# Kernel optimization log

Measured on AMD Instinct MI355X. Metric: run time of the kernel, lower is better.

Reference implementation:

```python
import jax, jax.numpy as jnp
import numpy as np

N_NODES = 20000
N_EDGES = 320000
IN_F = 16
OUT_F = 16
EDGE_DIM = 16
EDGE_HID = 64
BN_EPS = 1e-5


def setup_inputs() -> dict:
    key = jax.random.key(0)
    ks = jax.random.split(key, 12)
    inp = {
        "h_neigh": jax.random.normal(ks[0], (N_NODES, IN_F), dtype=jnp.float32),
        "h_self": jax.random.normal(ks[1], (N_NODES, IN_F), dtype=jnp.float32),
        "edge_features": jax.random.normal(ks[2], (N_EDGES, EDGE_DIM), dtype=jnp.float32),
        "src": jax.random.randint(ks[3], (N_EDGES,), 0, N_NODES),
        "dst": jax.random.randint(ks[4], (N_EDGES,), 0, N_NODES),
        # params (xavier-ish scale)
        "W_self": jax.random.normal(ks[5], (IN_F, OUT_F), dtype=jnp.float32) * (2.0 / (IN_F + OUT_F)) ** 0.5,
        "bn_gamma": jnp.ones((OUT_F,), dtype=jnp.float32),
        "bn_beta": jnp.zeros((OUT_F,), dtype=jnp.float32),
        "We1": jax.random.normal(ks[6], (EDGE_DIM, EDGE_HID), dtype=jnp.float32) * (2.0 / (EDGE_DIM + EDGE_HID)) ** 0.5,
        "be1": jnp.zeros((EDGE_HID,), dtype=jnp.float32),
        "We2": jax.random.normal(ks[7], (EDGE_HID, IN_F * OUT_F), dtype=jnp.float32) * (2.0 / (EDGE_HID + IN_F * OUT_F)) ** 0.5,
        "be2": jnp.zeros((IN_F * OUT_F,), dtype=jnp.float32),
    }
    return inp


def reference(h_neigh, h_self, edge_features, src, dst,
              W_self, bn_gamma, bn_beta, We1, be1, We2, be2):
    n_nodes = h_self.shape[0]
    in_f, out_f = W_self.shape
    # edge MLP -> per-edge weight matrix [E, in_f, out_f]
    eh = jax.nn.relu(edge_features @ We1 + be1)
    edge_w = (eh @ We2 + be2).reshape(-1, in_f, out_f)
    # gather src features, per-edge matvec, scatter-sum to dst
    # (sum over in_f commutes with the edge sum-reduce, matching
    #  update_all(u_mul_e, sum) followed by .sum(dim=1))
    msg = jnp.einsum('ei,eio->eo', h_neigh[src], edge_w)  # [E, out_f]
    neigh = jax.ops.segment_sum(msg, dst, num_segments=n_nodes)  # [N, out_f]
    # fc_self: Linear(no bias) -> BatchNorm1d (training stats) -> tanh
    y = h_self @ W_self
    mu = y.mean(axis=0)
    var = y.var(axis=0)
    y = (y - mu) / jnp.sqrt(var + BN_EPS) * bn_gamma + bn_beta
    y = jnp.tanh(y)
    z = jax.nn.relu(y + neigh)
    z_norm = jnp.linalg.norm(z, axis=1, keepdims=True)
    z_norm = jnp.where(z_norm == 0, jnp.ones_like(z_norm), z_norm)
    return z / z_norm
```

## Files before the change

kernel.cpp:

```cpp
#include <hip/hip_runtime.h>
#include <hip/hip_bf16.h>
#include <math.h>

#define NN 20000
#define NE 320000
#define BN_EPS 1e-5f
#define CAP 48
#define CNTP 16

#define MSG_BYTES   (NE * 16 * 4)
#define ELIST_OFF   MSG_BYTES
#define ELIST_BYTES (NN * CAP * 4)
#define CNT_OFF     (ELIST_OFF + ELIST_BYTES)
#define CNT_BYTES   (NN * CNTP * 4)
#define BNACC_OFF   (CNT_OFF + CNT_BYTES)
#define Y_OFF       (BNACC_OFF + 128)
#define ZERO_OFF    CNT_OFF
#define ZERO_BYTES  (CNT_BYTES + 128)

typedef __bf16 bf16x8 __attribute__((ext_vector_type(8)));
typedef float  f32x4  __attribute__((ext_vector_type(4)));

union BF8 { bf16x8 v; unsigned short us[8]; unsigned int ui[4]; };

__device__ __forceinline__ unsigned short f2bf(float f) {
    unsigned int u = __builtin_bit_cast(unsigned int, f);
    u += 0x7FFFu + ((u >> 16) & 1u);
    return (unsigned short)(u >> 16);
}
__device__ __forceinline__ float bf2f(unsigned short s) {
    unsigned int u = ((unsigned int)s) << 16;
    return __builtin_bit_cast(float, u);
}
__device__ __forceinline__ unsigned int pack2bf(float a, float b) {
    return (unsigned int)f2bf(a) | ((unsigned int)f2bf(b) << 16);
}

__global__ __launch_bounds__(256, 4) void edge_kernel(
    const float* __restrict__ h_neigh, const float* __restrict__ efeat,
    const int* __restrict__ src, const int* __restrict__ dst,
    const float* __restrict__ We1, const float* __restrict__ be1,
    const float* __restrict__ We2, const float* __restrict__ be2,
    float* __restrict__ msgb, int* __restrict__ elist,
    int* __restrict__ cntp,
    const float* __restrict__ h_self, const float* __restrict__ Wsf,
    float* __restrict__ y, float* __restrict__ bnacc)
{
    __shared__ __align__(16) unsigned short A3sw[16 * 2 * 64 * 8];
    __shared__ float red[4][32];

    const int t = threadIdx.x;

    {
        const float4* W2v = (const float4*)We2;
#pragma unroll
        for (int it = 0; it < 16; it++) {
            int c4 = t + 256 * it;
            float4 w = W2v[c4];
            int f = c4 * 4;
            int h = f >> 8, c = f & 255;
            int mb = c >> 4, kb = h >> 5, hh = h & 31, co = c & 15;
            int base = ((mb * 2 + kb) * 64 + (hh >> 3) * 16) * 8 + (hh & 7);
            A3sw[base + (co + 0) * 8] = f2bf(w.x);
            A3sw[base + (co + 1) * 8] = f2bf(w.y);
            A3sw[base + (co + 2) * 8] = f2bf(w.z);
            A3sw[base + (co + 3) * 8] = f2bf(w.w);
        }
    }

    for (int i = (int)blockIdx.x * 256 + t; i < NE; i += (int)gridDim.x * 256) {
        int d0 = dst[i];
        int k0 = atomicAdd(&cntp[d0 * CNTP], 1);
        if (k0 < CAP) elist[d0 * CAP + k0] = i;
    }
    __syncthreads();

    const int L = t & 63, wv = t >> 6;
    const int lo16 = L & 15, q = L >> 4;
    const int qc = q & 1;
    const bool qlow = (q < 2);
    const bool qhi1 = ((q >> 1) != 0);

    BF8 w1h[4], w1l[4];
#pragma unroll
    for (int c = 0; c < 4; c++) {
#pragma unroll
        for (int j = 0; j < 8; j++) {
            float w;
            if (q < 2)                 w = We1[(q * 8 + j) * 64 + c * 16 + lo16];
            else if (q == 2 && j == 0) w = be1[c * 16 + lo16];
            else                       w = 0.f;
            unsigned short h = f2bf(w);
            w1h[c].us[j] = h;
            w1l[c].us[j] = f2bf(w - bf2f(h));
        }
    }

    BF8 be2T;
#pragma unroll
    for (int j = 0; j < 8; j++) {
        float bv = be2[(qc * 8 + j) * 16 + lo16];
        be2T.us[j] = qlow ? f2bf(bv) : (unsigned short)0;
    }

    const int addrA = (((q & 1) * 2 + 0) * 16 + lo16) * 4;
    const int addrB = (((q & 1) * 2 + 1) * 16 + lo16) * 4;

    const int NT = NE / 64;
    int bt = blockIdx.x;
    {
        int e = bt * 64 + wv * 16 + lo16;
        int se = src[e];

        while (true) {
            int btn = bt + gridDim.x;
            bool hn = btn < NT;
            int en = 0, sen = 0;
            if (hn) {
                en = btn * 64 + wv * 16 + lo16;
                sen = src[en];
            }

            float xr[16];
            {
                const float4* xp = (const float4*)(h_neigh + (size_t)se * 16);
#pragma unroll
                for (int k4 = 0; k4 < 4; k4++) {
                    float4 a = xp[k4];
                    xr[k4*4+0] = a.x; xr[k4*4+1] = a.y; xr[k4*4+2] = a.z; xr[k4*4+3] = a.w;
                }
            }

            BF8 a2h, a2l;
            {
                const float4* ep = (const float4*)(efeat + (size_t)e * 16 + qc * 8);
                float4 e0 = ep[0], e1 = ep[1];
                float ev[8] = {e0.x, e0.y, e0.z, e0.w, e1.x, e1.y, e1.z, e1.w};
#pragma unroll
                for (int j = 0; j < 8; j++) {
                    if (qlow) {
                        unsigned short h = f2bf(ev[j]);
                        a2h.us[j] = h;
                        a2l.us[j] = f2bf(ev[j] - bf2f(h));
                    } else {
                        a2h.us[j] = (q == 2 && j == 0) ? (unsigned short)0x3F80 : (unsigned short)0;
                        a2l.us[j] = 0;
                    }
                }
            }

            float vch[4][4];
#pragma unroll
            for (int c = 0; c < 4; c++) {
                f32x4 c2 = {0.f, 0.f, 0.f, 0.f};
                c2 = __builtin_amdgcn_mfma_f32_16x16x32_bf16(w1h[c].v, a2h.v, c2, 0, 0, 0);
                c2 = __builtin_amdgcn_mfma_f32_16x16x32_bf16(w1l[c].v, a2h.v, c2, 0, 0, 0);
                c2 = __builtin_amdgcn_mfma_f32_16x16x32_bf16(w1h[c].v, a2l.v, c2, 0, 0, 0);
#pragma unroll
                for (int r = 0; r < 4; r++) vch[c][r] = fmaxf(c2[r], 0.f);
            }

            unsigned int dwH[4][2], dwL[4][2];
#pragma unroll
            for (int c = 0; c < 4; c++) {
#pragma unroll
                for (int d = 0; d < 2; d++) {
                    float va = vch[c][2*d], vb = vch[c][2*d+1];
                    unsigned short ha = f2bf(va), hb = f2bf(vb);
                    dwH[c][d] = (unsigned int)ha | ((unsigned int)hb << 16);
                    dwL[c][d] = pack2bf(va - bf2f(ha), vb - bf2f(hb));
                }
            }

            BF8 b3h[2], b3l[2];
#pragma unroll
            for (int kb = 0; kb < 2; kb++) {
#pragma unroll
                for (int tt = 0; tt < 4; tt++) {
                    int d = tt & 1;
                    int addr = (tt >> 1) ? addrB : addrA;
                    int h0 = __builtin_amdgcn_ds_bpermute(addr, (int)dwH[kb*2+0][d]);
                    int h1 = __builtin_amdgcn_ds_bpermute(addr, (int)dwH[kb*2+1][d]);
                    int l0 = __builtin_amdgcn_ds_bpermute(addr, (int)dwL[kb*2+0][d]);
                    int l1 = __builtin_amdgcn_ds_bpermute(addr, (int)dwL[kb*2+1][d]);
                    b3h[kb].ui[tt] = (unsigned int)(qhi1 ? h1 : h0);
                    b3l[kb].ui[tt] = (unsigned int)(qhi1 ? l1 : l0);
                }
            }

            BF8 xT;
#pragma unroll
            for (int j = 0; j < 8; j++)
                xT.us[j] = qlow ? f2bf(xr[qc * 8 + j]) : (unsigned short)0;
            f32x4 msg = {0.f, 0.f, 0.f, 0.f};
            msg = __builtin_amdgcn_mfma_f32_16x16x32_bf16(be2T.v, xT.v, msg, 0, 0, 0);

#pragma unroll 4
            for (int mb = 0; mb < 16; mb++) {
                bf16x8 a3a = *(const bf16x8*)&A3sw[((mb * 2 + 0) * 64 + L) * 8];
                bf16x8 a3b = *(const bf16x8*)&A3sw[((mb * 2 + 1) * 64 + L) * 8];
                f32x4 acc = {0.f, 0.f, 0.f, 0.f};
                acc = __builtin_amdgcn_mfma_f32_16x16x32_bf16(a3a, b3h[0].v, acc, 0, 0, 0);
                acc = __builtin_amdgcn_mfma_f32_16x16x32_bf16(a3b, b3h[1].v, acc, 0, 0, 0);
                acc = __builtin_amdgcn_mfma_f32_16x16x32_bf16(a3a, b3l[0].v, acc, 0, 0, 0);
                acc = __builtin_amdgcn_mfma_f32_16x16x32_bf16(a3b, b3l[1].v, acc, 0, 0, 0);
                float xm = xr[mb];
                msg[0] += xm * acc[0];
                msg[1] += xm * acc[1];
                msg[2] += xm * acc[2];
                msg[3] += xm * acc[3];
            }

            *(float4*)(msgb + (size_t)e * 16 + q * 4) =
                make_float4(msg[0], msg[1], msg[2], msg[3]);

            if (!hn) break;
            bt = btn; e = en; se = sen;
        }
    }

    int sb = (int)blockIdx.x - 945;
    if (sb >= 0 && sb < 79) {
        int n = sb * 256 + t;
        bool act = (n < NN);
        float hv[16], yv[16];
        if (act) {
            const float4* h4 = (const float4*)(h_self + (size_t)n * 16);
#pragma unroll
            for (int k = 0; k < 4; k++) {
                float4 a = h4[k];
                hv[4*k+0] = a.x; hv[4*k+1] = a.y; hv[4*k+2] = a.z; hv[4*k+3] = a.w;
            }
        } else {
#pragma unroll
            for (int i = 0; i < 16; i++) hv[i] = 0.f;
        }
#pragma unroll
        for (int o = 0; o < 16; o++) {
            float a = 0.f;
#pragma unroll
            for (int i = 0; i < 16; i++) a += hv[i] * Wsf[i*16 + o];
            yv[o] = a;
        }
        if (act) {
            float4* y4 = (float4*)(y + (size_t)n * 16);
#pragma unroll
            for (int k = 0; k < 4; k++)
                y4[k] = make_float4(yv[4*k+0], yv[4*k+1], yv[4*k+2], yv[4*k+3]);
        }
        int lane = t & 63;
#pragma unroll
        for (int o = 0; o < 16; o++) {
            float a = act ? yv[o] : 0.f;
            float b = act ? yv[o]*yv[o] : 0.f;
#pragma unroll
            for (int off = 32; off > 0; off >>= 1) {
                a += __shfl_down(a, off);
                b += __shfl_down(b, off);
            }
            if (lane == 0) { red[wv][o] = a; red[wv][16 + o] = b; }
        }
        __syncthreads();
        if (t < 32) {
            float s = red[0][t] + red[1][t] + red[2][t] + red[3][t];
            atomicAdd(&bnacc[t], s);
        }
    }
}

__global__ __launch_bounds__(256) void final_kernel(
    const float* __restrict__ msgb, const int* __restrict__ elist,
    const int* __restrict__ cntp, const int* __restrict__ dst,
    const float* __restrict__ y, const float* __restrict__ bnacc,
    const float* __restrict__ gamma, const float* __restrict__ beta,
    float* __restrict__ out)
{
    int tb = blockIdx.x * 256 + threadIdx.x;
    int n = tb >> 2, c = tb & 3;
    if (n >= NN) return;

    int deg = cntp[n * CNTP];
    const float4* m4 = (const float4*)msgb;

    float ax = 0.f, ay = 0.f, az = 0.f, aw = 0.f;
    if (deg <= CAP) {
        const int* el = elist + n * CAP;
        int k = 0;
        for (; k + 4 <= deg; k += 4) {
            int e0 = el[k], e1 = el[k+1], e2 = el[k+2], e3 = el[k+3];
            float4 a0 = m4[(size_t)e0*4 + c];
            float4 a1 = m4[(size_t)e1*4 + c];
            float4 a2 = m4[(size_t)e2*4 + c];
            float4 a3 = m4[(size_t)e3*4 + c];
            ax += (a0.x + a1.x) + (a2.x + a3.x);
            ay += (a0.y + a1.y) + (a2.y + a3.y);
            az += (a0.z + a1.z) + (a2.z + a3.z);
            aw += (a0.w + a1.w) + (a2.w + a3.w);
        }
        for (; k < deg; k++) {
            int e0 = el[k];
            float4 a0 = m4[(size_t)e0*4 + c];
            ax += a0.x; ay += a0.y; az += a0.z; aw += a0.w;
        }
    } else {
        for (int e0 = 0; e0 < NE; e0++) {
            if (dst[e0] == n) {
                float4 a0 = m4[(size_t)e0*4 + c];
                ax += a0.x; ay += a0.y; az += a0.z; aw += a0.w;
            }
        }
    }

    float4 yv4 = ((const float4*)y)[(size_t)n * 4 + c];
    float yv[4] = {yv4.x, yv4.y, yv4.z, yv4.w};
    float nb[4] = {ax, ay, az, aw};

    const float inv_n = 1.f / (float)NN;
    float z[4];
    float ss = 0.f;
#pragma unroll
    for (int r = 0; r < 4; r++) {
        int o = c * 4 + r;
        float mu  = bnacc[o] * inv_n;
        float var = bnacc[16 + o] * inv_n - mu * mu;
        float inv = rsqrtf(var + BN_EPS);
        float yy  = (yv[r] - mu) * inv * gamma[o] + beta[o];
        float tt  = tanhf(yy);
        float zz  = fmaxf(tt + nb[r], 0.f);
        z[r] = zz;
        ss += zz * zz;
    }
    ss += __shfl_xor(ss, 1);
    ss += __shfl_xor(ss, 2);
    float nrm = sqrtf(ss);
    if (nrm == 0.f) nrm = 1.f;
    float rr = 1.f / nrm;
    *(float4*)(out + (size_t)n * 16 + c * 4) =
        make_float4(z[0]*rr, z[1]*rr, z[2]*rr, z[3]*rr);
}

extern "C" void kernel_launch(void* const* d_in, const int* in_sizes, int n_in,
                              void* d_out, int out_size, void* d_ws, size_t ws_size,
                              hipStream_t stream) {
    const float* h_neigh = (const float*)d_in[0];
    const float* h_self  = (const float*)d_in[1];
    const float* efeat   = (const float*)d_in[2];
    const int*   src     = (const int*)d_in[3];
    const int*   dst     = (const int*)d_in[4];
    const float* W_self  = (const float*)d_in[5];
    const float* gamma   = (const float*)d_in[6];
    const float* beta    = (const float*)d_in[7];
    const float* We1     = (const float*)d_in[8];
    const float* be1     = (const float*)d_in[9];
    const float* We2     = (const float*)d_in[10];
    const float* be2     = (const float*)d_in[11];
    float* out = (float*)d_out;

    char* ws = (char*)d_ws;
    float* msgb  = (float*)ws;
    int*   elist = (int*)(ws + ELIST_OFF);
    int*   cntp  = (int*)(ws + CNT_OFF);
    float* bnacc = (float*)(ws + BNACC_OFF);
    float* y     = (float*)(ws + Y_OFF);

    hipMemsetAsync(ws + ZERO_OFF, 0, ZERO_BYTES, stream);

    edge_kernel<<<1024, 256, 0, stream>>>(
        h_neigh, efeat, src, dst, We1, be1, We2, be2,
        msgb, elist, cntp,
        h_self, W_self, y, bnacc);
    final_kernel<<<(NN * 4 + 255) / 256, 256, 0, stream>>>(
        msgb, elist, cntp, dst, y, bnacc, gamma, beta, out);
}
```

Baseline: 156.3 us.

## Double edge-kernel block size, use per-wave grid-stride loop, use native bf16 conversions

The edge kernel moves from 256 to 512 threads per block, raising launch bounds to 8 waves per SIMD target, so each block's one-time LDS staging of the We2 matrix is shared by twice as many waves. The main loop changes from a per-block tile loop with software prefetch of the next src index to a simple per-wave grid-stride loop over 16-edge groups, which drops the prefetch. Bucketing by destination becomes one edge per thread, since 1024×512 threads cover all edges. The BN-statistics blocks are remapped to the last blocks. Manual bf16 round/extend bit tricks are replaced by native __bf16 casts, which may map to hardware conversion instructions. The tighter launch bound risks register spills, and losing the prefetch may expose gather latency.

```diff
diff --git a/kernel.cpp b/kernel.cpp
--- a/kernel.cpp
+++ b/kernel.cpp
@@ -24,19 +24,17 @@
 union BF8 { bf16x8 v; unsigned short us[8]; unsigned int ui[4]; };
 
 __device__ __forceinline__ unsigned short f2bf(float f) {
-    unsigned int u = __builtin_bit_cast(unsigned int, f);
-    u += 0x7FFFu + ((u >> 16) & 1u);
-    return (unsigned short)(u >> 16);
+    __bf16 h = (__bf16)f;
+    return __builtin_bit_cast(unsigned short, h);
 }
 __device__ __forceinline__ float bf2f(unsigned short s) {
-    unsigned int u = ((unsigned int)s) << 16;
-    return __builtin_bit_cast(float, u);
+    return (float)__builtin_bit_cast(__bf16, s);
 }
 __device__ __forceinline__ unsigned int pack2bf(float a, float b) {
     return (unsigned int)f2bf(a) | ((unsigned int)f2bf(b) << 16);
 }
 
-__global__ __launch_bounds__(256, 4) void edge_kernel(
+__global__ __launch_bounds__(512, 8) void edge_kernel(
     const float* __restrict__ h_neigh, const float* __restrict__ efeat,
     const int* __restrict__ src, const int* __restrict__ dst,
     const float* __restrict__ We1, const float* __restrict__ be1,
@@ -47,15 +45,15 @@
     float* __restrict__ y, float* __restrict__ bnacc)
 {
     __shared__ __align__(16) unsigned short A3sw[16 * 2 * 64 * 8];
-    __shared__ float red[4][32];
+    __shared__ float red[8][32];
 
     const int t = threadIdx.x;
 
     {
         const float4* W2v = (const float4*)We2;
 #pragma unroll
-        for (int it = 0; it < 16; it++) {
-            int c4 = t + 256 * it;
+        for (int it = 0; it < 8; it++) {
+            int c4 = t + 512 * it;
             float4 w = W2v[c4];
             int f = c4 * 4;
             int h = f >> 8, c = f & 255;
@@ -68,10 +66,13 @@
         }
     }
 
-    for (int i = (int)blockIdx.x * 256 + t; i < NE; i += (int)gridDim.x * 256) {
-        int d0 = dst[i];
-        int k0 = atomicAdd(&cntp[d0 * CNTP], 1);
-        if (k0 < CAP) elist[d0 * CAP + k0] = i;
+    {
+        int i = (int)blockIdx.x * 512 + t;
+        if (i < NE) {
+            int d0 = dst[i];
+            int k0 = atomicAdd(&cntp[d0 * CNTP], 1);
+            if (k0 < CAP) elist[d0 * CAP + k0] = i;
+        }
     }
     __syncthreads();
 
@@ -106,122 +107,109 @@
     const int addrA = (((q & 1) * 2 + 0) * 16 + lo16) * 4;
     const int addrB = (((q & 1) * 2 + 1) * 16 + lo16) * 4;
 
-    const int NT = NE / 64;
-    int bt = blockIdx.x;
-    {
-        int e = bt * 64 + wv * 16 + lo16;
+    const int NG = NE / 16;
+    const int NW = (int)gridDim.x * 8;
+    for (int g = (int)blockIdx.x * 8 + wv; g < NG; g += NW) {
+        int e = g * 16 + lo16;
         int se = src[e];
 
-        while (true) {
-            int btn = bt + gridDim.x;
-            bool hn = btn < NT;
-            int en = 0, sen = 0;
-            if (hn) {
-                en = btn * 64 + wv * 16 + lo16;
-                sen = src[en];
-            }
-
-            float xr[16];
-            {
-                const float4* xp = (const float4*)(h_neigh + (size_t)se * 16);
-#pragma unroll
-                for (int k4 = 0; k4 < 4; k4++) {
-                    float4 a = xp[k4];
-                    xr[k4*4+0] = a.x; xr[k4*4+1] = a.y; xr[k4*4+2] = a.z; xr[k4*4+3] = a.w;
+        float xr[16];
+        {
+            const float4* xp = (const float4*)(h_neigh + (size_t)se * 16);
+#pragma unroll
+            for (int k4 = 0; k4 < 4; k4++) {
+                float4 a = xp[k4];
+                xr[k4*4+0] = a.x; xr[k4*4+1] = a.y; xr[k4*4+2] = a.z; xr[k4*4+3] = a.w;
+            }
+        }
+
+        BF8 a2h, a2l;
+        {
+            const float4* ep = (const float4*)(efeat + (size_t)e * 16 + qc * 8);
+            float4 e0 = ep[0], e1 = ep[1];
+            float ev[8] = {e0.x, e0.y, e0.z, e0.w, e1.x, e1.y, e1.z, e1.w};
+#pragma unroll
+            for (int j = 0; j < 8; j++) {
+                if (qlow) {
+                    unsigned short h = f2bf(ev[j]);
+                    a2h.us[j] = h;
+                    a2l.us[j] = f2bf(ev[j] - bf2f(h));
+                } else {
+                    a2h.us[j] = (q == 2 && j == 0) ? (unsigned short)0x3F80 : (unsigned short)0;
+                    a2l.us[j] = 0;
                 }
             }
-
-            BF8 a2h, a2l;
-            {
-                const float4* ep = (const float4*)(efeat + (size_t)e * 16 + qc * 8);
-                float4 e0 = ep[0], e1 = ep[1];
-                float ev[8] = {e0.x, e0.y, e0.z, e0.w, e1.x, e1.y, e1.z, e1.w};
-#pragma unroll
-                for (int j = 0; j < 8; j++) {
-                    if (qlow) {
-                        unsigned short h = f2bf(ev[j]);
-                        a2h.us[j] = h;
-                        a2l.us[j] = f2bf(ev[j] - bf2f(h));
-                    } else {
-                        a2h.us[j] = (q == 2 && j == 0) ? (unsigned short)0x3F80 : (unsigned short)0;
-                        a2l.us[j] = 0;
-                    }
-                }
-            }
-
-            float vch[4][4];
-#pragma unroll
-            for (int c = 0; c < 4; c++) {
-                f32x4 c2 = {0.f, 0.f, 0.f, 0.f};
-                c2 = __builtin_amdgcn_mfma_f32_16x16x32_bf16(w1h[c].v, a2h.v, c2, 0, 0, 0);
-                c2 = __builtin_amdgcn_mfma_f32_16x16x32_bf16(w1l[c].v, a2h.v, c2, 0, 0, 0);
-                c2 = __builtin_amdgcn_mfma_f32_16x16x32_bf16(w1h[c].v, a2l.v, c2, 0, 0, 0);
-#pragma unroll
-                for (int r = 0; r < 4; r++) vch[c][r] = fmaxf(c2[r], 0.f);
-            }
-
-            unsigned int dwH[4][2], dwL[4][2];
-#pragma unroll
-            for (int c = 0; c < 4; c++) {
-#pragma unroll
-                for (int d = 0; d < 2; d++) {
-                    float va = vch[c][2*d], vb = vch[c][2*d+1];
-                    unsigned short ha = f2bf(va), hb = f2bf(vb);
-                    dwH[c][d] = (unsigned int)ha | ((unsigned int)hb << 16);
-                    dwL[c][d] = pack2bf(va - bf2f(ha), vb - bf2f(hb));
-                }
-            }
-
-            BF8 b3h[2], b3l[2];
-#pragma unroll
-            for (int kb = 0; kb < 2; kb++) {
-#pragma unroll
-                for (int tt = 0; tt < 4; tt++) {
-                    int d = tt & 1;
-                    int addr = (tt >> 1) ? addrB : addrA;
-                    int h0 = __builtin_amdgcn_ds_bpermute(addr, (int)dwH[kb*2+0][d]);
-                    int h1 = __builtin_amdgcn_ds_bpermute(addr, (int)dwH[kb*2+1][d]);
-                    int l0 = __builtin_amdgcn_ds_bpermute(addr, (int)dwL[kb*2+0][d]);
-                    int l1 = __builtin_amdgcn_ds_bpermute(addr, (int)dwL[kb*2+1][d]);
-                    b3h[kb].ui[tt] = (unsigned int)(qhi1 ? h1 : h0);
-                    b3l[kb].ui[tt] = (unsigned int)(qhi1 ? l1 : l0);
-                }
-            }
-
-            BF8 xT;
-#pragma unroll
-            for (int j = 0; j < 8; j++)
-                xT.us[j] = qlow ? f2bf(xr[qc * 8 + j]) : (unsigned short)0;
-            f32x4 msg = {0.f, 0.f, 0.f, 0.f};
-            msg = __builtin_amdgcn_mfma_f32_16x16x32_bf16(be2T.v, xT.v, msg, 0, 0, 0);
+        }
+
+        float vch[4][4];
+#pragma unroll
+        for (int c = 0; c < 4; c++) {
+            f32x4 c2 = {0.f, 0.f, 0.f, 0.f};
+            c2 = __builtin_amdgcn_mfma_f32_16x16x32_bf16(w1h[c].v, a2h.v, c2, 0, 0, 0);
+            c2 = __builtin_amdgcn_mfma_f32_16x16x32_bf16(w1l[c].v, a2h.v, c2, 0, 0, 0);
+            c2 = __builtin_amdgcn_mfma_f32_16x16x32_bf16(w1h[c].v, a2l.v, c2, 0, 0, 0);
+#pragma unroll
+            for (int r = 0; r < 4; r++) vch[c][r] = fmaxf(c2[r], 0.f);
+        }
+
+        unsigned int dwH[4][2], dwL[4][2];
+#pragma unroll
+        for (int c = 0; c < 4; c++) {
+#pragma unroll
+            for (int d = 0; d < 2; d++) {
+                float va = vch[c][2*d], vb = vch[c][2*d+1];
+                unsigned short ha = f2bf(va), hb = f2bf(vb);
+                dwH[c][d] = (unsigned int)ha | ((unsigned int)hb << 16);
+                dwL[c][d] = pack2bf(va - bf2f(ha), vb - bf2f(hb));
+            }
+        }
+
+        BF8 b3h[2], b3l[2];
+#pragma unroll
+        for (int kb = 0; kb < 2; kb++) {
+#pragma unroll
+            for (int tt = 0; tt < 4; tt++) {
+                int d = tt & 1;
+                int addr = (tt >> 1) ? addrB : addrA;
+                int h0 = __builtin_amdgcn_ds_bpermute(addr, (int)dwH[kb*2+0][d]);
+                int h1 = __builtin_amdgcn_ds_bpermute(addr, (int)dwH[kb*2+1][d]);
+                int l0 = __builtin_amdgcn_ds_bpermute(addr, (int)dwL[kb*2+0][d]);
+                int l1 = __builtin_amdgcn_ds_bpermute(addr, (int)dwL[kb*2+1][d]);
+                b3h[kb].ui[tt] = (unsigned int)(qhi1 ? h1 : h0);
+                b3l[kb].ui[tt] = (unsigned int)(qhi1 ? l1 : l0);
+            }
+        }
+
+        BF8 xT;
+#pragma unroll
+        for (int j = 0; j < 8; j++)
+            xT.us[j] = qlow ? f2bf(xr[qc * 8 + j]) : (unsigned short)0;
+        f32x4 msg = {0.f, 0.f, 0.f, 0.f};
+        msg = __builtin_amdgcn_mfma_f32_16x16x32_bf16(be2T.v, xT.v, msg, 0, 0, 0);
 
 #pragma unroll 4
-            for (int mb = 0; mb < 16; mb++) {
-                bf16x8 a3a = *(const bf16x8*)&A3sw[((mb * 2 + 0) * 64 + L) * 8];
-                bf16x8 a3b = *(const bf16x8*)&A3sw[((mb * 2 + 1) * 64 + L) * 8];
-                f32x4 acc = {0.f, 0.f, 0.f, 0.f};
-                acc = __builtin_amdgcn_mfma_f32_16x16x32_bf16(a3a, b3h[0].v, acc, 0, 0, 0);
-                acc = __builtin_amdgcn_mfma_f32_16x16x32_bf16(a3b, b3h[1].v, acc, 0, 0, 0);
-                acc = __builtin_amdgcn_mfma_f32_16x16x32_bf16(a3a, b3l[0].v, acc, 0, 0, 0);
-                acc = __builtin_amdgcn_mfma_f32_16x16x32_bf16(a3b, b3l[1].v, acc, 0, 0, 0);
-                float xm = xr[mb];
-                msg[0] += xm * acc[0];
-                msg[1] += xm * acc[1];
-                msg[2] += xm * acc[2];
-                msg[3] += xm * acc[3];
-            }
-
-            *(float4*)(msgb + (size_t)e * 16 + q * 4) =
-                make_float4(msg[0], msg[1], msg[2], msg[3]);
-
-            if (!hn) break;
-            bt = btn; e = en; se = sen;
-        }
-    }
-
-    int sb = (int)blockIdx.x - 945;
-    if (sb >= 0 && sb < 79) {
-        int n = sb * 256 + t;
+        for (int mb = 0; mb < 16; mb++) {
+            bf16x8 a3a = *(const bf16x8*)&A3sw[((mb * 2 + 0) * 64 + L) * 8];
+            bf16x8 a3b = *(const bf16x8*)&A3sw[((mb * 2 + 1) * 64 + L) * 8];
+            f32x4 acc = {0.f, 0.f, 0.f, 0.f};
+            acc = __builtin_amdgcn_mfma_f32_16x16x32_bf16(a3a, b3h[0].v, acc, 0, 0, 0);
+            acc = __builtin_amdgcn_mfma_f32_16x16x32_bf16(a3b, b3h[1].v, acc, 0, 0, 0);
+            acc = __builtin_amdgcn_mfma_f32_16x16x32_bf16(a3a, b3l[0].v, acc, 0, 0, 0);
+            acc = __builtin_amdgcn_mfma_f32_16x16x32_bf16(a3b, b3l[1].v, acc, 0, 0, 0);
+            float xm = xr[mb];
+            msg[0] += xm * acc[0];
+            msg[1] += xm * acc[1];
+            msg[2] += xm * acc[2];
+            msg[3] += xm * acc[3];
+        }
+
+        *(float4*)(msgb + (size_t)e * 16 + q * 4) =
+            make_float4(msg[0], msg[1], msg[2], msg[3]);
+    }
+
+    int sb = (int)blockIdx.x - 984;
+    if (sb >= 0) {
+        int n = sb * 512 + t;
         bool act = (n < NN);
         float hv[16], yv[16];
         if (act) {
@@ -262,7 +250,9 @@
         }
         __syncthreads();
         if (t < 32) {
-            float s = red[0][t] + red[1][t] + red[2][t] + red[3][t];
+            float s = 0.f;
+#pragma unroll
+            for (int w = 0; w < 8; w++) s += red[w][t];
             atomicAdd(&bnacc[t], s);
         }
     }
@@ -365,7 +355,7 @@
 
     hipMemsetAsync(ws + ZERO_OFF, 0, ZERO_BYTES, stream);
 
-    edge_kernel<<<1024, 256, 0, stream>>>(
+    edge_kernel<<<1024, 512, 0, stream>>>(
         h_neigh, efeat, src, dst, We1, be1, We2, be2,
         msgb, elist, cntp,
         h_self, W_self, y, bnacc);
```

Result: slower. 196.9 us (+26.0%).

## Switch edge MLP MFMAs from split-bf16 to single fp16

Applied to the files above, without the earlier changes.

Replaces the hi/lo bf16 splitting, which took three or four MFMAs per product plus extra bpermutes, with single fp16 MFMAs. This roughly halves the matrix work and the cross-lane shuffles in the edge MLP. The first four We2 tiles are also held in registers instead of being reloaded from LDS on every iteration. fp16 has a narrower range and gives less precision than the split-bf16 scheme, and the register-cached tiles raise register pressure.

```diff
diff --git a/kernel.cpp b/kernel.cpp
--- a/kernel.cpp
+++ b/kernel.cpp
@@ -18,22 +18,17 @@
 #define ZERO_OFF    CNT_OFF
 #define ZERO_BYTES  (CNT_BYTES + 128)
 
-typedef __bf16 bf16x8 __attribute__((ext_vector_type(8)));
-typedef float  f32x4  __attribute__((ext_vector_type(4)));
-
-union BF8 { bf16x8 v; unsigned short us[8]; unsigned int ui[4]; };
-
-__device__ __forceinline__ unsigned short f2bf(float f) {
-    unsigned int u = __builtin_bit_cast(unsigned int, f);
-    u += 0x7FFFu + ((u >> 16) & 1u);
-    return (unsigned short)(u >> 16);
-}
-__device__ __forceinline__ float bf2f(unsigned short s) {
-    unsigned int u = ((unsigned int)s) << 16;
-    return __builtin_bit_cast(float, u);
-}
-__device__ __forceinline__ unsigned int pack2bf(float a, float b) {
-    return (unsigned int)f2bf(a) | ((unsigned int)f2bf(b) << 16);
+typedef _Float16 f16x8 __attribute__((ext_vector_type(8)));
+typedef float    f32x4 __attribute__((ext_vector_type(4)));
+
+union H8 { f16x8 v; unsigned short us[8]; unsigned int ui[4]; };
+
+__device__ __forceinline__ unsigned short f2h(float f) {
+    _Float16 h = (_Float16)f;
+    return __builtin_bit_cast(unsigned short, h);
+}
+__device__ __forceinline__ unsigned int pack2h(float a, float b) {
+    return (unsigned int)f2h(a) | ((unsigned int)f2h(b) << 16);
 }
 
 __global__ __launch_bounds__(256, 4) void edge_kernel(
@@ -61,10 +56,10 @@
             int h = f >> 8, c = f & 255;
             int mb = c >> 4, kb = h >> 5, hh = h & 31, co = c & 15;
             int base = ((mb * 2 + kb) * 64 + (hh >> 3) * 16) * 8 + (hh & 7);
-            A3sw[base + (co + 0) * 8] = f2bf(w.x);
-            A3sw[base + (co + 1) * 8] = f2bf(w.y);
-            A3sw[base + (co + 2) * 8] = f2bf(w.z);
-            A3sw[base + (co + 3) * 8] = f2bf(w.w);
+            A3sw[base + (co + 0) * 8] = f2h(w.x);
+            A3sw[base + (co + 1) * 8] = f2h(w.y);
+            A3sw[base + (co + 2) * 8] = f2h(w.z);
+            A3sw[base + (co + 3) * 8] = f2h(w.w);
         }
     }
 
@@ -81,7 +76,14 @@
     const bool qlow = (q < 2);
     const bool qhi1 = ((q >> 1) != 0);
 
-    BF8 w1h[4], w1l[4];
+    H8 a3r[4][2];
+#pragma unroll
+    for (int mb = 0; mb < 4; mb++) {
+        a3r[mb][0].v = *(const f16x8*)&A3sw[((mb * 2 + 0) * 64 + L) * 8];
+        a3r[mb][1].v = *(const f16x8*)&A3sw[((mb * 2 + 1) * 64 + L) * 8];
+    }
+
+    H8 w1[4];
 #pragma unroll
     for (int c = 0; c < 4; c++) {
 #pragma unroll
@@ -90,17 +92,15 @@
             if (q < 2)                 w = We1[(q * 8 + j) * 64 + c * 16 + lo16];
             else if (q == 2 && j == 0) w = be1[c * 16 + lo16];
             else                       w = 0.f;
-            unsigned short h = f2bf(w);
-            w1h[c].us[j] = h;
-            w1l[c].us[j] = f2bf(w - bf2f(h));
-        }
-    }
-
-    BF8 be2T;
+            w1[c].us[j] = f2h(w);
+        }
+    }
+
+    H8 be2T;
 #pragma unroll
     for (int j = 0; j < 8; j++) {
         float bv = be2[(qc * 8 + j) * 16 + lo16];
-        be2T.us[j] = qlow ? f2bf(bv) : (unsigned short)0;
+        be2T.us[j] = qlow ? f2h(bv) : (unsigned short)0;
     }
 
     const int addrA = (((q & 1) * 2 + 0) * 16 + lo16) * 4;
@@ -131,7 +131,7 @@
                 }
             }
 
-            BF8 a2h, a2l;
+            H8 a2;
             {
                 const float4* ep = (const float4*)(efeat + (size_t)e * 16 + qc * 8);
                 float4 e0 = ep[0], e1 = ep[1];
@@ -139,12 +139,9 @@
 #pragma unroll
                 for (int j = 0; j < 8; j++) {
                     if (qlow) {
-                        unsigned short h = f2bf(ev[j]);
-                        a2h.us[j] = h;
-                        a2l.us[j] = f2bf(ev[j] - bf2f(h));
+                        a2.us[j] = f2h(ev[j]);
                     } else {
-                        a2h.us[j] = (q == 2 && j == 0) ? (unsigned short)0x3F80 : (unsigned short)0;
-                        a2l.us[j] = 0;
+                        a2.us[j] = (q == 2 && j == 0) ? (unsigned short)0x3C00 : (unsigned short)0;
                     }
                 }
             }
@@ -153,57 +150,57 @@
 #pragma unroll
             for (int c = 0; c < 4; c++) {
                 f32x4 c2 = {0.f, 0.f, 0.f, 0.f};
-                c2 = __builtin_amdgcn_mfma_f32_16x16x32_bf16(w1h[c].v, a2h.v, c2, 0, 0, 0);
-                c2 = __builtin_amdgcn_mfma_f32_16x16x32_bf16(w1l[c].v, a2h.v, c2, 0, 0, 0);
-                c2 = __builtin_amdgcn_mfma_f32_16x16x32_bf16(w1h[c].v, a2l.v, c2, 0, 0, 0);
+                c2 = __builtin_amdgcn_mfma_f32_16x16x32_f16(w1[c].v, a2.v, c2, 0, 0, 0);
 #pragma unroll
                 for (int r = 0; r < 4; r++) vch[c][r] = fmaxf(c2[r], 0.f);
             }
 
-            unsigned int dwH[4][2], dwL[4][2];
+            unsigned int dw[4][2];
 #pragma unroll
             for (int c = 0; c < 4; c++) {
 #pragma unroll
-                for (int d = 0; d < 2; d++) {
-                    float va = vch[c][2*d], vb = vch[c][2*d+1];
-                    unsigned short ha = f2bf(va), hb = f2bf(vb);
-                    dwH[c][d] = (unsigned int)ha | ((unsigned int)hb << 16);
-                    dwL[c][d] = pack2bf(va - bf2f(ha), vb - bf2f(hb));
-                }
-            }
-
-            BF8 b3h[2], b3l[2];
+                for (int d = 0; d < 2; d++)
+                    dw[c][d] = pack2h(vch[c][2*d], vch[c][2*d+1]);
+            }
+
+            H8 b3[2];
 #pragma unroll
             for (int kb = 0; kb < 2; kb++) {
 #pragma unroll
                 for (int tt = 0; tt < 4; tt++) {
                     int d = tt & 1;
                     int addr = (tt >> 1) ? addrB : addrA;
-                    int h0 = __builtin_amdgcn_ds_bpermute(addr, (int)dwH[kb*2+0][d]);
-                    int h1 = __builtin_amdgcn_ds_bpermute(addr, (int)dwH[kb*2+1][d]);
-                    int l0 = __builtin_amdgcn_ds_bpermute(addr, (int)dwL[kb*2+0][d]);
-                    int l1 = __builtin_amdgcn_ds_bpermute(addr, (int)dwL[kb*2+1][d]);
-                    b3h[kb].ui[tt] = (unsigned int)(qhi1 ? h1 : h0);
-                    b3l[kb].ui[tt] = (unsigned int)(qhi1 ? l1 : l0);
+                    int h0 = __builtin_amdgcn_ds_bpermute(addr, (int)dw[kb*2+0][d]);
+                    int h1 = __builtin_amdgcn_ds_bpermute(addr, (int)dw[kb*2+1][d]);
+                    b3[kb].ui[tt] = (unsigned int)(qhi1 ? h1 : h0);
                 }
             }
 
-            BF8 xT;
+            H8 xT;
 #pragma unroll
             for (int j = 0; j < 8; j++)
-                xT.us[j] = qlow ? f2bf(xr[qc * 8 + j]) : (unsigned short)0;
+                xT.us[j] = qlow ? f2h(xr[qc * 8 + j]) : (unsigned short)0;
             f32x4 msg = {0.f, 0.f, 0.f, 0.f};
-            msg = __builtin_amdgcn_mfma_f32_16x16x32_bf16(be2T.v, xT.v, msg, 0, 0, 0);
-
+            msg = __builtin_amdgcn_mfma_f32_16x16x32_f16(be2T.v, xT.v, msg, 0, 0, 0);
+
+#pragma unroll
+            for (int mb = 0; mb < 4; mb++) {
+                f32x4 acc = {0.f, 0.f, 0.f, 0.f};
+                acc = __builtin_amdgcn_mfma_f32_16x16x32_f16(a3r[mb][0].v, b3[0].v, acc, 0, 0, 0);
+                acc = __builtin_amdgcn_mfma_f32_16x16x32_f16(a3r[mb][1].v, b3[1].v, acc, 0, 0, 0);
+                float xm = xr[mb];
+                msg[0] += xm * acc[0];
+                msg[1] += xm * acc[1];
+                msg[2] += xm * acc[2];
+                msg[3] += xm * acc[3];
+            }
 #pragma unroll 4
-            for (int mb = 0; mb < 16; mb++) {
-                bf16x8 a3a = *(const bf16x8*)&A3sw[((mb * 2 + 0) * 64 + L) * 8];
-                bf16x8 a3b = *(const bf16x8*)&A3sw[((mb * 2 + 1) * 64 + L) * 8];
+            for (int mb = 4; mb < 16; mb++) {
+                f16x8 a3a = *(const f16x8*)&A3sw[((mb * 2 + 0) * 64 + L) * 8];
+                f16x8 a3b = *(const f16x8*)&A3sw[((mb * 2 + 1) * 64 + L) * 8];
                 f32x4 acc = {0.f, 0.f, 0.f, 0.f};
-                acc = __builtin_amdgcn_mfma_f32_16x16x32_bf16(a3a, b3h[0].v, acc, 0, 0, 0);
-                acc = __builtin_amdgcn_mfma_f32_16x16x32_bf16(a3b, b3h[1].v, acc, 0, 0, 0);
-                acc = __builtin_amdgcn_mfma_f32_16x16x32_bf16(a3a, b3l[0].v, acc, 0, 0, 0);
-                acc = __builtin_amdgcn_mfma_f32_16x16x32_bf16(a3b, b3l[1].v, acc, 0, 0, 0);
+                acc = __builtin_amdgcn_mfma_f32_16x16x32_f16(a3a, b3[0].v, acc, 0, 0, 0);
+                acc = __builtin_amdgcn_mfma_f32_16x16x32_f16(a3b, b3[1].v, acc, 0, 0, 0);
                 float xm = xr[mb];
                 msg[0] += xm * acc[0];
                 msg[1] += xm * acc[1];
```

After: 148.5 us. 5.0% less time.
